# Optimization experiments

Hardware: AMD Instinct MI355X
Metric: run time of the kernel (lower is better)

The kernel has to match this reference:

```python
import jax, jax.numpy as jnp
import numpy as np
from jax import lax

P = 5  # patch_size ('shape' init arg)
EPS = 1e-06


def _box_mean(x, p=P):
    # valid 5x5 mean filter, 1 channel: [B,1,H,W] -> [B,1,H-p+1,W-p+1]
    k = jnp.full((1, 1, p, p), 1.0 / (p * p), dtype=x.dtype)
    return lax.conv_general_dilated(
        x, k, window_strides=(1, 1), padding='VALID',
        dimension_numbers=('NCHW', 'OIHW', 'NCHW'))


def _center(x, p=P):
    # conv2d with the ones_mask (single 1 at center) == center crop
    h = p // 2
    return x[:, :, h:-h, h:-h]


def setup_inputs() -> dict:
    key = jax.random.key(0)
    k1, k2, k3 = jax.random.split(key, 3)
    B, C, H, W = 8, 1, 1024, 1024
    x = jax.random.normal(k1, (B, C, H, W), dtype=jnp.float32)
    y = jax.random.normal(k2, (B, C, H, W), dtype=jnp.float32)
    mask = jax.random.uniform(k3, (B, C, H, W), dtype=jnp.float32)
    return {"x": x, "y": y, "mask": mask}


def reference(x, y, mask):
    # channels == 1 path of YIQGNGCLoss.forward (mask is unused, as in source)
    dx = _center(x) - _box_mean(x)  # (E[x] at center) - local mean
    dy = _center(y) - _box_mean(y)
    c = _box_mean(dx * dy)                      # local covariance
    vx = _box_mean(dx * dx)                     # local variance of x
    vy = _box_mean(dy * dy)                     # local variance of y
    vv = jnp.sqrt(vx * vy)
    low = vv < EPS
    c = jnp.where(low, 0.0, c)
    vv = jnp.where(low, EPS, vv)
    corr = jnp.clip(c / vv, 0.0, 1.0)
    return (corr, vv, c)
```

## Files before the change

kernel.cpp:

```cpp
#include <hip/hip_runtime.h>
#include <math.h>

#define H 1024
#define W 1024
#define OH 1016
#define OW 1016
#define BH 16
#define NBANDS 64
#define NCHUNK 5
#define CSTR 248
#define NIMG 8
#define NWG (NBANDS*NCHUNK*NIMG)
#define EPS 1e-6f
#define EPS2 1e-12f
#define INV25 (1.0f/25.0f)


__device__ __forceinline__ float4 ld4(const float* p){ return *reinterpret_cast<const float4*>(p); }
__device__ __forceinline__ void st4(float* p, float4 v){ *reinterpret_cast<float4*>(p) = v; }

__global__ __launch_bounds__(64, 2)
void yiq_gngc_coop(const float* __restrict__ x, const float* __restrict__ y,
                   float* __restrict__ out, long long Nper)
{
    __shared__ __align__(16) float4 ring[5][2][64];
    const int t = (int)threadIdx.x;

    const int wg  = (int)blockIdx.x;
    const int nid = (wg & 7) * (NWG / 8) + (wg >> 3);
    const int band  = nid % NBANDS;
    const int rest  = nid / NBANDS;
    const int chunk = rest % NCHUNK;
    const int b     = rest / NCHUNK;

    const int jc = chunk * CSTR;
    const int j0 = jc + 4 * t;
    const int j0L = (j0 > W - 4) ? (W - 4) : j0;
    const bool dostore = (t <= 61) && (j0 <= OW - 4);
    const int i0 = band * BH;
    const float* xb = x + (size_t)b * (H * W) + j0L;
    const float* yb = y + (size_t)b * (H * W) + j0L;

    float csx[4], csy[4];
    float cp1[8], cp2[8], cp3[8];
    #pragma unroll
    for (int k = 0; k < 4; ++k) { csx[k] = 0.f; csy[k] = 0.f; }
    #pragma unroll
    for (int k = 0; k < 8; ++k) { cp1[k] = 0.f; cp2[k] = 0.f; cp3[k] = 0.f; }

    #pragma unroll
    for (int r = 0; r < 5; ++r) {
        float4 vx = ld4(xb + (size_t)(i0 + r) * W);
        float4 vy = ld4(yb + (size_t)(i0 + r) * W);
        csx[0] += vx.x; csx[1] += vx.y; csx[2] += vx.z; csx[3] += vx.w;
        csy[0] += vy.x; csy[1] += vy.y; csy[2] += vy.z; csy[3] += vy.w;
    }

    {
        float4 z = make_float4(0.f, 0.f, 0.f, 0.f);
        ring[4][0][t] = z; ring[4][1][t] = z;
    }

#define COMPUTE_D(dn, cs, c4)                                              \
    {                                                                      \
        float w4 = __shfl_down(cs[0], 1), w5 = __shfl_down(cs[1], 1);      \
        float w6 = __shfl_down(cs[2], 1), w7 = __shfl_down(cs[3], 1);      \
        float ce2 = __shfl_down(c4.x, 1), ce3 = __shfl_down(c4.y, 1);      \
        float m = cs[1] + cs[2] + cs[3];                                   \
        dn[0] = c4.z - (cs[0] + m + w4) * INV25;                           \
        dn[1] = c4.w - (m + w4 + w5) * INV25;                              \
        dn[2] = ce2 - (cs[2] + cs[3] + w4 + w5 + w6) * INV25;              \
        dn[3] = ce3 - (cs[3] + w4 + w5 + w6 + w7) * INV25;                 \
    }

    #pragma unroll
    for (int pr = 0; pr < 4; ++pr) {
        float4 xc = ld4(xb + (size_t)(i0 + pr + 2) * W);
        float4 yc = ld4(yb + (size_t)(i0 + pr + 2) * W);
        float4 nx = ld4(xb + (size_t)(i0 + pr + 5) * W);
        float4 ox = ld4(xb + (size_t)(i0 + pr) * W);
        float4 ny = ld4(yb + (size_t)(i0 + pr + 5) * W);
        float4 oy = ld4(yb + (size_t)(i0 + pr) * W);

        float dxn[4], dyn[4];
        COMPUTE_D(dxn, csx, xc);
        COMPUTE_D(dyn, csy, yc);
        float dhx[4], dhy[4];
        #pragma unroll
        for (int m = 0; m < 4; ++m) { dhx[m] = __shfl_down(dxn[m], 1); dhy[m] = __shfl_down(dyn[m], 1); }

        ring[pr][0][t] = make_float4(dxn[0], dxn[1], dxn[2], dxn[3]);
        ring[pr][1][t] = make_float4(dyn[0], dyn[1], dyn[2], dyn[3]);

        #pragma unroll
        for (int k = 0; k < 4; ++k) {
            cp1[k] += dxn[k] * dyn[k];  cp1[4 + k] += dhx[k] * dhy[k];
            cp2[k] += dxn[k] * dxn[k];  cp2[4 + k] += dhx[k] * dhx[k];
            cp3[k] += dyn[k] * dyn[k];  cp3[4 + k] += dhy[k] * dhy[k];
        }
        csx[0] += nx.x - ox.x; csx[1] += nx.y - ox.y; csx[2] += nx.z - ox.z; csx[3] += nx.w - ox.w;
        csy[0] += ny.x - oy.x; csy[1] += ny.y - oy.y; csy[2] += ny.z - oy.z; csy[3] += ny.w - oy.w;
    }

    float* ob = out + (size_t)b * ((size_t)OH * OW) + j0;
    int s = 4;

    #pragma unroll 4
    for (int it = 0; it < BH; ++it) {
        const int i = i0 + it;
        if (i >= OH) break;
        const bool slide = (it < BH - 1) && (i < OH - 1);

        float4 xc = ld4(xb + (size_t)(i + 6) * W);
        float4 yc = ld4(yb + (size_t)(i + 6) * W);
        float4 nx, ox, ny, oy;
        if (slide) {
            nx = ld4(xb + (size_t)(i + 9) * W);
            ox = ld4(xb + (size_t)(i + 4) * W);
            ny = ld4(yb + (size_t)(i + 9) * W);
            oy = ld4(yb + (size_t)(i + 4) * W);
        }

        float4 orx = ring[s][0][t];
        float4 ory = ring[s][1][t];
        float ohx0 = __shfl_down(orx.x, 1), ohx1 = __shfl_down(orx.y, 1);
        float ohx2 = __shfl_down(orx.z, 1), ohx3 = __shfl_down(orx.w, 1);
        float ohy0 = __shfl_down(ory.x, 1), ohy1 = __shfl_down(ory.y, 1);
        float ohy2 = __shfl_down(ory.z, 1), ohy3 = __shfl_down(ory.w, 1);

        float dxn[4], dyn[4];
        COMPUTE_D(dxn, csx, xc);
        COMPUTE_D(dyn, csy, yc);
        float dhx[4], dhy[4];
        #pragma unroll
        for (int m = 0; m < 4; ++m) { dhx[m] = __shfl_down(dxn[m], 1); dhy[m] = __shfl_down(dyn[m], 1); }

        ring[s][0][t] = make_float4(dxn[0], dxn[1], dxn[2], dxn[3]);
        ring[s][1][t] = make_float4(dyn[0], dyn[1], dyn[2], dyn[3]);

        float odx[8] = {orx.x, orx.y, orx.z, orx.w, ohx0, ohx1, ohx2, ohx3};
        float ody[8] = {ory.x, ory.y, ory.z, ory.w, ohy0, ohy1, ohy2, ohy3};
        float ndx[8] = {dxn[0], dxn[1], dxn[2], dxn[3], dhx[0], dhx[1], dhx[2], dhx[3]};
        float ndy[8] = {dyn[0], dyn[1], dyn[2], dyn[3], dhy[0], dhy[1], dhy[2], dhy[3]};
        #pragma unroll
        for (int k = 0; k < 8; ++k) {
            cp1[k] += ndx[k] * ndy[k] - odx[k] * ody[k];
            cp2[k] += ndx[k] * ndx[k] - odx[k] * odx[k];
            cp3[k] += ndy[k] * ndy[k] - ody[k] * ody[k];
        }

        if (dostore) {
            float co[4], vv[4], cc[4];
            #pragma unroll
            for (int q = 0; q < 4; ++q) {
                float c_ = (cp1[q] + cp1[q+1] + cp1[q+2] + cp1[q+3] + cp1[q+4]) * INV25;
                float vx = (cp2[q] + cp2[q+1] + cp2[q+2] + cp2[q+3] + cp2[q+4]) * INV25;
                float vy = (cp3[q] + cp3[q+1] + cp3[q+2] + cp3[q+3] + cp3[q+4]) * INV25;
                float sp = vx * vy;
                bool lo  = sp < EPS2;
                float r  = __builtin_amdgcn_rsqf(sp);
                float cr = c_ * r;
                cr = cr < 0.f ? 0.f : (cr > 1.f ? 1.f : cr);
                co[q] = lo ? 0.f : cr;
                vv[q] = lo ? EPS : sp * r;
                cc[q] = lo ? 0.f : c_;
            }
            float* o = ob + (size_t)i * OW;
            st4(o,            make_float4(co[0], co[1], co[2], co[3]));
            st4(o + Nper,     make_float4(vv[0], vv[1], vv[2], vv[3]));
            st4(o + 2 * Nper, make_float4(cc[0], cc[1], cc[2], cc[3]));
        }

        if (slide) {
            csx[0] += nx.x - ox.x; csx[1] += nx.y - ox.y; csx[2] += nx.z - ox.z; csx[3] += nx.w - ox.w;
            csy[0] += ny.x - oy.x; csy[1] += ny.y - oy.y; csy[2] += ny.z - oy.z; csy[3] += ny.w - oy.w;
        }
        s = (s == 4) ? 0 : s + 1;
    }
}

extern "C" void kernel_launch(void* const* d_in, const int* in_sizes, int n_in,
                              void* d_out, int out_size, void* d_ws, size_t ws_size,
                              hipStream_t stream) {
    const float* x = (const float*)d_in[0];
    const float* y = (const float*)d_in[1];
    float* out = (float*)d_out;
    const long long Nper = (long long)out_size / 3;
    yiq_gngc_coop<<<dim3(NWG), dim3(64), 0, stream>>>(x, y, out, Nper);
}
```

Baseline: 54.57 us.

## Replace repeated global row reloads with prefix-sum and raw-row LDS rings

The vertical 5-row column sum now comes from a running prefix sum: each new row is loaded from global memory once, and the window sum is the current prefix minus a prefix kept in an LDS ring. The centre row also comes from a small LDS ring of raw rows. Before, each output row reloaded the centre, incoming and outgoing rows from global memory, so every input row was read about three times; now each is read once. In exchange the kernel does more LDS traffic and uses more LDS per workgroup. The running prefix sum can also lose float precision across the band.

```diff
diff --git a/kernel.cpp b/kernel.cpp
--- a/kernel.cpp
+++ b/kernel.cpp
@@ -18,12 +18,17 @@
 
 __device__ __forceinline__ float4 ld4(const float* p){ return *reinterpret_cast<const float4*>(p); }
 __device__ __forceinline__ void st4(float* p, float4 v){ *reinterpret_cast<float4*>(p) = v; }
+__device__ __forceinline__ float4 f4add(float4 a, float4 b){
+    return make_float4(a.x+b.x, a.y+b.y, a.z+b.z, a.w+b.w);
+}
 
 __global__ __launch_bounds__(64, 2)
-void yiq_gngc_coop(const float* __restrict__ x, const float* __restrict__ y,
-                   float* __restrict__ out, long long Nper)
+void yiq_gngc_pfx(const float* __restrict__ x, const float* __restrict__ y,
+                  float* __restrict__ out, long long Nper)
 {
-    __shared__ __align__(16) float4 ring[5][2][64];
+    __shared__ __align__(16) float4 dring[5][2][64];
+    __shared__ __align__(16) float4 pring[6][2][64];
+    __shared__ __align__(16) float4 rring[3][2][64];
     const int t = (int)threadIdx.x;
 
     const int wg  = (int)blockIdx.x;
@@ -41,25 +46,11 @@
     const float* xb = x + (size_t)b * (H * W) + j0L;
     const float* yb = y + (size_t)b * (H * W) + j0L;
 
-    float csx[4], csy[4];
+    float4 Px = make_float4(0.f, 0.f, 0.f, 0.f);
+    float4 Py = make_float4(0.f, 0.f, 0.f, 0.f);
     float cp1[8], cp2[8], cp3[8];
     #pragma unroll
-    for (int k = 0; k < 4; ++k) { csx[k] = 0.f; csy[k] = 0.f; }
-    #pragma unroll
     for (int k = 0; k < 8; ++k) { cp1[k] = 0.f; cp2[k] = 0.f; cp3[k] = 0.f; }
-
-    #pragma unroll
-    for (int r = 0; r < 5; ++r) {
-        float4 vx = ld4(xb + (size_t)(i0 + r) * W);
-        float4 vy = ld4(yb + (size_t)(i0 + r) * W);
-        csx[0] += vx.x; csx[1] += vx.y; csx[2] += vx.z; csx[3] += vx.w;
-        csy[0] += vy.x; csy[1] += vy.y; csy[2] += vy.z; csy[3] += vy.w;
-    }
-
-    {
-        float4 z = make_float4(0.f, 0.f, 0.f, 0.f);
-        ring[4][0][t] = z; ring[4][1][t] = z;
-    }
 
 #define COMPUTE_D(dn, cs, c4)                                              \
     {                                                                      \
@@ -73,24 +64,46 @@
         dn[3] = ce3 - (cs[3] + w4 + w5 + w6 + w7) * INV25;                 \
     }
 
+    {
+        float4 z = make_float4(0.f, 0.f, 0.f, 0.f);
+        dring[4][0][t] = z; dring[4][1][t] = z;
+    }
+
     #pragma unroll
-    for (int pr = 0; pr < 4; ++pr) {
-        float4 xc = ld4(xb + (size_t)(i0 + pr + 2) * W);
-        float4 yc = ld4(yb + (size_t)(i0 + pr + 2) * W);
-        float4 nx = ld4(xb + (size_t)(i0 + pr + 5) * W);
-        float4 ox = ld4(xb + (size_t)(i0 + pr) * W);
-        float4 ny = ld4(yb + (size_t)(i0 + pr + 5) * W);
-        float4 oy = ld4(yb + (size_t)(i0 + pr) * W);
+    for (int r = 0; r < 4; ++r) {
+        float4 vx = ld4(xb + (size_t)(i0 + r) * W);
+        float4 vy = ld4(yb + (size_t)(i0 + r) * W);
+        Px = f4add(Px, vx); Py = f4add(Py, vy);
+        pring[r][0][t] = Px; pring[r][1][t] = Py;
+        rring[r % 3][0][t] = vx; rring[r % 3][1][t] = vy;
+    }
+
+    #pragma unroll
+    for (int r = 4; r < 8; ++r) {
+        float4 vx = ld4(xb + (size_t)(i0 + r) * W);
+        float4 vy = ld4(yb + (size_t)(i0 + r) * W);
+        Px = f4add(Px, vx); Py = f4add(Py, vy);
+        pring[r % 6][0][t] = Px; pring[r % 6][1][t] = Py;
+        rring[r % 3][0][t] = vx; rring[r % 3][1][t] = vy;
+
+        const int m = r - 4;
+        float4 cx = rring[(m + 2) % 3][0][t];
+        float4 cy = rring[(m + 2) % 3][1][t];
+        float4 pox, poy;
+        if (m == 0) { pox = make_float4(0.f,0.f,0.f,0.f); poy = pox; }
+        else        { pox = pring[m - 1][0][t]; poy = pring[m - 1][1][t]; }
+        float csx[4] = {Px.x - pox.x, Px.y - pox.y, Px.z - pox.z, Px.w - pox.w};
+        float csy[4] = {Py.x - poy.x, Py.y - poy.y, Py.z - poy.z, Py.w - poy.w};
 
         float dxn[4], dyn[4];
-        COMPUTE_D(dxn, csx, xc);
-        COMPUTE_D(dyn, csy, yc);
+        COMPUTE_D(dxn, csx, cx);
+        COMPUTE_D(dyn, csy, cy);
         float dhx[4], dhy[4];
         #pragma unroll
-        for (int m = 0; m < 4; ++m) { dhx[m] = __shfl_down(dxn[m], 1); dhy[m] = __shfl_down(dyn[m], 1); }
-
-        ring[pr][0][t] = make_float4(dxn[0], dxn[1], dxn[2], dxn[3]);
-        ring[pr][1][t] = make_float4(dyn[0], dyn[1], dyn[2], dyn[3]);
+        for (int q = 0; q < 4; ++q) { dhx[q] = __shfl_down(dxn[q], 1); dhy[q] = __shfl_down(dyn[q], 1); }
+
+        dring[m][0][t] = make_float4(dxn[0], dxn[1], dxn[2], dxn[3]);
+        dring[m][1][t] = make_float4(dyn[0], dyn[1], dyn[2], dyn[3]);
 
         #pragma unroll
         for (int k = 0; k < 4; ++k) {
@@ -98,45 +111,54 @@
             cp2[k] += dxn[k] * dxn[k];  cp2[4 + k] += dhx[k] * dhx[k];
             cp3[k] += dyn[k] * dyn[k];  cp3[4 + k] += dhy[k] * dhy[k];
         }
-        csx[0] += nx.x - ox.x; csx[1] += nx.y - ox.y; csx[2] += nx.z - ox.z; csx[3] += nx.w - ox.w;
-        csy[0] += ny.x - oy.x; csy[1] += ny.y - oy.y; csy[2] += ny.z - oy.z; csy[3] += ny.w - oy.w;
+    }
+
+    {
+        float4 vx = ld4(xb + (size_t)(i0 + 8) * W);
+        float4 vy = ld4(yb + (size_t)(i0 + 8) * W);
+        Px = f4add(Px, vx); Py = f4add(Py, vy);
+        pring[8 % 6][0][t] = Px; pring[8 % 6][1][t] = Py;
+        rring[8 % 3][0][t] = vx; rring[8 % 3][1][t] = vy;
     }
 
     float* ob = out + (size_t)b * ((size_t)OH * OW) + j0;
-    int s = 4;
 
     #pragma unroll 4
     for (int it = 0; it < BH; ++it) {
         const int i = i0 + it;
         if (i >= OH) break;
         const bool slide = (it < BH - 1) && (i < OH - 1);
-
-        float4 xc = ld4(xb + (size_t)(i + 6) * W);
-        float4 yc = ld4(yb + (size_t)(i + 6) * W);
-        float4 nx, ox, ny, oy;
+        const int sp = (it + 3) % 6;
+        const int sr = it % 3;
+        const int s  = (it + 4) % 5;
+
+        float4 nx, ny;
         if (slide) {
             nx = ld4(xb + (size_t)(i + 9) * W);
-            ox = ld4(xb + (size_t)(i + 4) * W);
             ny = ld4(yb + (size_t)(i + 9) * W);
-            oy = ld4(yb + (size_t)(i + 4) * W);
-        }
-
-        float4 orx = ring[s][0][t];
-        float4 ory = ring[s][1][t];
+        }
+
+        float4 pox = pring[sp][0][t], poy = pring[sp][1][t];
+        float4 cx  = rring[sr][0][t], cy  = rring[sr][1][t];
+        float4 orx = dring[s][0][t],  ory = dring[s][1][t];
+
+        float csx[4] = {Px.x - pox.x, Px.y - pox.y, Px.z - pox.z, Px.w - pox.w};
+        float csy[4] = {Py.x - poy.x, Py.y - poy.y, Py.z - poy.z, Py.w - poy.w};
+
         float ohx0 = __shfl_down(orx.x, 1), ohx1 = __shfl_down(orx.y, 1);
         float ohx2 = __shfl_down(orx.z, 1), ohx3 = __shfl_down(orx.w, 1);
         float ohy0 = __shfl_down(ory.x, 1), ohy1 = __shfl_down(ory.y, 1);
         float ohy2 = __shfl_down(ory.z, 1), ohy3 = __shfl_down(ory.w, 1);
 
         float dxn[4], dyn[4];
-        COMPUTE_D(dxn, csx, xc);
-        COMPUTE_D(dyn, csy, yc);
+        COMPUTE_D(dxn, csx, cx);
+        COMPUTE_D(dyn, csy, cy);
         float dhx[4], dhy[4];
         #pragma unroll
-        for (int m = 0; m < 4; ++m) { dhx[m] = __shfl_down(dxn[m], 1); dhy[m] = __shfl_down(dyn[m], 1); }
-
-        ring[s][0][t] = make_float4(dxn[0], dxn[1], dxn[2], dxn[3]);
-        ring[s][1][t] = make_float4(dyn[0], dyn[1], dyn[2], dyn[3]);
+        for (int q = 0; q < 4; ++q) { dhx[q] = __shfl_down(dxn[q], 1); dhy[q] = __shfl_down(dyn[q], 1); }
+
+        dring[s][0][t] = make_float4(dxn[0], dxn[1], dxn[2], dxn[3]);
+        dring[s][1][t] = make_float4(dyn[0], dyn[1], dyn[2], dyn[3]);
 
         float odx[8] = {orx.x, orx.y, orx.z, orx.w, ohx0, ohx1, ohx2, ohx3};
         float ody[8] = {ory.x, ory.y, ory.z, ory.w, ohy0, ohy1, ohy2, ohy3};
@@ -156,13 +178,13 @@
                 float c_ = (cp1[q] + cp1[q+1] + cp1[q+2] + cp1[q+3] + cp1[q+4]) * INV25;
                 float vx = (cp2[q] + cp2[q+1] + cp2[q+2] + cp2[q+3] + cp2[q+4]) * INV25;
                 float vy = (cp3[q] + cp3[q+1] + cp3[q+2] + cp3[q+3] + cp3[q+4]) * INV25;
-                float sp = vx * vy;
-                bool lo  = sp < EPS2;
-                float r  = __builtin_amdgcn_rsqf(sp);
-                float cr = c_ * r;
+                float sq = vx * vy;
+                bool lo  = sq < EPS2;
+                float rr = __builtin_amdgcn_rsqf(sq);
+                float cr = c_ * rr;
                 cr = cr < 0.f ? 0.f : (cr > 1.f ? 1.f : cr);
                 co[q] = lo ? 0.f : cr;
-                vv[q] = lo ? EPS : sp * r;
+                vv[q] = lo ? EPS : sq * rr;
                 cc[q] = lo ? 0.f : c_;
             }
             float* o = ob + (size_t)i * OW;
@@ -172,10 +194,10 @@
         }
 
         if (slide) {
-            csx[0] += nx.x - ox.x; csx[1] += nx.y - ox.y; csx[2] += nx.z - ox.z; csx[3] += nx.w - ox.w;
-            csy[0] += ny.x - oy.x; csy[1] += ny.y - oy.y; csy[2] += ny.z - oy.z; csy[3] += ny.w - oy.w;
-        }
-        s = (s == 4) ? 0 : s + 1;
+            Px = f4add(Px, nx); Py = f4add(Py, ny);
+            pring[sp][0][t] = Px; pring[sp][1][t] = Py;
+            rring[sr][0][t] = nx; rring[sr][1][t] = ny;
+        }
     }
 }
 
@@ -186,5 +208,5 @@
     const float* y = (const float*)d_in[1];
     float* out = (float*)d_out;
     const long long Nper = (long long)out_size / 3;
-    yiq_gngc_coop<<<dim3(NWG), dim3(64), 0, stream>>>(x, y, out, Nper);
+    yiq_gngc_pfx<<<dim3(NWG), dim3(64), 0, stream>>>(x, y, out, Nper);
 }
```

New measurement: 55.90 us. 1.02x slower.

## Double-buffer row loads via async global-to-LDS copies and use nontemporal stores

Applied to the files above, without the earlier changes.

Replaces the per-iteration global register loads in the main sliding loop with global_load_lds async copies into a two-stage LDS buffer. Each iteration prefetches the next row's six vectors and waits with an explicit vmcnt. Output stores become nontemporal to avoid polluting cache. The loop is no longer unrolled, and the slide update now always runs on clamped rows. The explicit waitcnt may interact badly with the nontemporal stores, since stores also count toward vmcnt on some targets, and no barrier orders the LDS read against the async write within the wave.

```diff
diff --git a/kernel.cpp b/kernel.cpp
--- a/kernel.cpp
+++ b/kernel.cpp
@@ -16,14 +16,25 @@
 #define INV25 (1.0f/25.0f)
 
 
+typedef float vfloat4 __attribute__((ext_vector_type(4)));
+
 __device__ __forceinline__ float4 ld4(const float* p){ return *reinterpret_cast<const float4*>(p); }
-__device__ __forceinline__ void st4(float* p, float4 v){ *reinterpret_cast<float4*>(p) = v; }
+__device__ __forceinline__ void st4nt(float* p, float4 v){
+    vfloat4 w; w.x = v.x; w.y = v.y; w.z = v.z; w.w = v.w;
+    __builtin_nontemporal_store(w, reinterpret_cast<vfloat4*>(p));
+}
+
+#define GLOAD_LDS16(g, l)                                                   \
+    __builtin_amdgcn_global_load_lds(                                       \
+        (const __attribute__((address_space(1))) void*)(g),                 \
+        (__attribute__((address_space(3))) void*)(l), 16, 0, 0)
 
 __global__ __launch_bounds__(64, 2)
-void yiq_gngc_coop(const float* __restrict__ x, const float* __restrict__ y,
-                   float* __restrict__ out, long long Nper)
+void yiq_gngc_async(const float* __restrict__ x, const float* __restrict__ y,
+                    float* __restrict__ out, long long Nper)
 {
     __shared__ __align__(16) float4 ring[5][2][64];
+    __shared__ __align__(16) float4 stage[2][6][64];
     const int t = (int)threadIdx.x;
 
     const int wg  = (int)blockIdx.x;
@@ -104,22 +115,42 @@
 
     float* ob = out + (size_t)b * ((size_t)OH * OW) + j0;
     int s = 4;
-
-    #pragma unroll 4
+    int cur = 0;
+
+    GLOAD_LDS16(xb + (size_t)(i0 + 6) * W, &stage[0][0][0]);
+    GLOAD_LDS16(yb + (size_t)(i0 + 6) * W, &stage[0][1][0]);
+    GLOAD_LDS16(xb + (size_t)(i0 + 9) * W, &stage[0][2][0]);
+    GLOAD_LDS16(xb + (size_t)(i0 + 4) * W, &stage[0][3][0]);
+    GLOAD_LDS16(yb + (size_t)(i0 + 9) * W, &stage[0][4][0]);
+    GLOAD_LDS16(yb + (size_t)(i0 + 4) * W, &stage[0][5][0]);
+
+    #pragma unroll 1
     for (int it = 0; it < BH; ++it) {
         const int i = i0 + it;
         if (i >= OH) break;
-        const bool slide = (it < BH - 1) && (i < OH - 1);
-
-        float4 xc = ld4(xb + (size_t)(i + 6) * W);
-        float4 yc = ld4(yb + (size_t)(i + 6) * W);
-        float4 nx, ox, ny, oy;
-        if (slide) {
-            nx = ld4(xb + (size_t)(i + 9) * W);
-            ox = ld4(xb + (size_t)(i + 4) * W);
-            ny = ld4(yb + (size_t)(i + 9) * W);
-            oy = ld4(yb + (size_t)(i + 4) * W);
-        }
+
+        {
+            int rc = i + 7;  rc = rc > H - 1 ? H - 1 : rc;
+            int rn = i + 10; rn = rn > H - 1 ? H - 1 : rn;
+            int ro = i + 5;  ro = ro > H - 1 ? H - 1 : ro;
+            const int nb = cur ^ 1;
+            GLOAD_LDS16(xb + (size_t)rc * W, &stage[nb][0][0]);
+            GLOAD_LDS16(yb + (size_t)rc * W, &stage[nb][1][0]);
+            GLOAD_LDS16(xb + (size_t)rn * W, &stage[nb][2][0]);
+            GLOAD_LDS16(xb + (size_t)ro * W, &stage[nb][3][0]);
+            GLOAD_LDS16(yb + (size_t)rn * W, &stage[nb][4][0]);
+            GLOAD_LDS16(yb + (size_t)ro * W, &stage[nb][5][0]);
+        }
+        __builtin_amdgcn_sched_barrier(0);
+        asm volatile("s_waitcnt vmcnt(6)" ::: "memory");
+        __builtin_amdgcn_sched_barrier(0);
+
+        float4 xc = stage[cur][0][t];
+        float4 yc = stage[cur][1][t];
+        float4 nx = stage[cur][2][t];
+        float4 ox = stage[cur][3][t];
+        float4 ny = stage[cur][4][t];
+        float4 oy = stage[cur][5][t];
 
         float4 orx = ring[s][0][t];
         float4 ory = ring[s][1][t];
@@ -166,15 +197,15 @@
                 cc[q] = lo ? 0.f : c_;
             }
             float* o = ob + (size_t)i * OW;
-            st4(o,            make_float4(co[0], co[1], co[2], co[3]));
-            st4(o + Nper,     make_float4(vv[0], vv[1], vv[2], vv[3]));
-            st4(o + 2 * Nper, make_float4(cc[0], cc[1], cc[2], cc[3]));
-        }
-
-        if (slide) {
-            csx[0] += nx.x - ox.x; csx[1] += nx.y - ox.y; csx[2] += nx.z - ox.z; csx[3] += nx.w - ox.w;
-            csy[0] += ny.x - oy.x; csy[1] += ny.y - oy.y; csy[2] += ny.z - oy.z; csy[3] += ny.w - oy.w;
-        }
+            st4nt(o,            make_float4(co[0], co[1], co[2], co[3]));
+            st4nt(o + Nper,     make_float4(vv[0], vv[1], vv[2], vv[3]));
+            st4nt(o + 2 * Nper, make_float4(cc[0], cc[1], cc[2], cc[3]));
+        }
+
+        csx[0] += nx.x - ox.x; csx[1] += nx.y - ox.y; csx[2] += nx.z - ox.z; csx[3] += nx.w - ox.w;
+        csy[0] += ny.x - oy.x; csy[1] += ny.y - oy.y; csy[2] += ny.z - oy.z; csy[3] += ny.w - oy.w;
+
+        cur ^= 1;
         s = (s == 4) ? 0 : s + 1;
     }
 }
@@ -186,5 +217,5 @@
     const float* y = (const float*)d_in[1];
     float* out = (float*)d_out;
     const long long Nper = (long long)out_size / 3;
-    yiq_gngc_coop<<<dim3(NWG), dim3(64), 0, stream>>>(x, y, out, Nper);
+    yiq_gngc_async<<<dim3(NWG), dim3(64), 0, stream>>>(x, y, out, Nper);
 }
```

New measurement: 59.42 us. 8.9% more time.
